# Kernel optimization log

Hardware: AMD Instinct MI355X
Metric: run time of the kernel (lower is better)

Reference implementation:

```python
import jax, jax.numpy as jnp
import numpy as np

B, T, D = 2, 4096, 512
H, W = 8, 32
HD = D // H            # 64
HIDDEN = 3 * D         # SwiGLU expansion = 3
SCALE = float(np.sqrt(HD))
EPS = 1e-5


def setup_inputs() -> dict:
    key = jax.random.key(0)
    ks = jax.random.split(key, 8)
    s = 0.02  # small init for weight matrices
    return {
        "x": jax.random.normal(ks[0], (B, T, D), dtype=jnp.float32),
        "pre_g": jnp.ones((D,), jnp.float32), "pre_b": jnp.zeros((D,), jnp.float32),
        "wq": jax.random.normal(ks[1], (D, D), jnp.float32) * s,
        "wkv": jax.random.normal(ks[2], (D, 2 * D), jnp.float32) * s,
        "wo": jax.random.normal(ks[3], (D, D), jnp.float32) * s,
        "attn_g": jnp.ones((D,), jnp.float32), "attn_b": jnp.zeros((D,), jnp.float32),
        "freqs": jax.random.normal(ks[4], (D,), jnp.float32) * 0.02,
        "phases": jnp.zeros((D,), jnp.float32),
        "amp": jnp.full((1,), 0.1, jnp.float32),
        "w_gate": jax.random.normal(ks[5], (D, HIDDEN), jnp.float32) * s,
        "w_val": jax.random.normal(ks[6], (D, HIDDEN), jnp.float32) * s,
        "w_proj": jax.random.normal(ks[7], (HIDDEN, D), jnp.float32) * s,
        "ffn_g": jnp.ones((D,), jnp.float32), "ffn_b": jnp.zeros((D,), jnp.float32),
    }


def _ln(x, g, b):
    mu = jnp.mean(x, axis=-1, keepdims=True)
    var = jnp.mean(jnp.square(x - mu), axis=-1, keepdims=True)
    return (x - mu) * jax.lax.rsqrt(var + EPS) * g + b


def _gather_window(z):
    # z: (B, T, H, C) -> nb: (B, T, W, H, C) with nb[:, t, w] = z[:, t-1-w] (zeros if t-1-w < 0)
    zp = jnp.pad(z, ((0, 0), (W, 0), (0, 0), (0, 0)))
    idx = jnp.arange(T)[:, None] + (W - 1) - jnp.arange(W)[None, :]  # (T, W), values in [0, T+W-1)
    return zp[:, idx]  # (B, T, W, H, C)


def reference(x, pre_g, pre_b, wq, wkv, wo, attn_g, attn_b,
              freqs, phases, amp, w_gate, w_val, w_proj, ffn_g, ffn_b):
    h = _ln(x, pre_g, pre_b)

    # ---- multi-head causal tension (sigmoid local attention) ----
    q = (h @ wq).reshape(B, T, H, HD)
    kv = (h @ wkv).reshape(B, T, H, 2 * HD)
    nb_kv = _gather_window(kv)                     # (B, T, W, H, 2*HD)
    nb_k, nb_v = nb_kv[..., :HD], nb_kv[..., HD:]
    tau = jax.nn.sigmoid(jnp.einsum('bthd,btwhd->bthw', q, nb_k) / SCALE)
    msg = jnp.einsum('bthw,btwhd->bthd', tau, nb_v).reshape(B, T, D)
    h = _ln(h + msg @ wo, attn_g, attn_b)

    # ---- oscillatory modulation ----
    pos = jnp.arange(T, dtype=jnp.float32)[:, None]  # (T, 1)
    mod = jnp.sin(pos * freqs + phases)              # (T, D)
    y = h * (1.0 + amp * mod)[None]

    # ---- SwiGLU FFN ----
    z = (jax.nn.silu(y @ w_gate) * (y @ w_val)) @ w_proj
    return _ln(y + z, ffn_g, ffn_b)
```

## Files before the change

kernel.cpp:

```cpp
#include <hip/hip_runtime.h>
#include <hip/hip_bf16.h>
#include <math.h>

#define T_LEN   4096
#define D_DIM   512
#define H_NUM   8
#define HD_DIM  64
#define W_WIN   32
#define HID_DIM 1536
#define M_ROWS  8192
#define QKV_LD  1536
#define BK 64

typedef __hip_bfloat16 bf16;
typedef __bf16  bf16x8 __attribute__((ext_vector_type(8)));
typedef float   f32x4  __attribute__((ext_vector_type(4)));

__device__ __forceinline__ float b2f(bf16 x) { return __bfloat162float(x); }
__device__ __forceinline__ bf16  f2b(float x){ return __float2bfloat16(x); }

__device__ __forceinline__ float rdP(const void* p, int i, bool f32) {
  return f32 ? ((const float*)p)[i] : b2f(((const bf16*)p)[i]);
}

__device__ __forceinline__ float wave_reduce_sum(float v) {
  #pragma unroll
  for (int off = 32; off; off >>= 1) v += __shfl_xor(v, off, 64);
  return v;
}

__device__ __forceinline__ bool detect_f32(const unsigned* __restrict__ x) {
  int lane = threadIdx.x & 63;
  int votes = 0;
  #pragma unroll
  for (int i = 0; i < 4; ++i) {
    unsigned e = (x[lane * 4 + i] >> 7) & 0xffu;
    votes += (e >= 90u && e <= 140u) ? 1 : 0;
  }
  float v = wave_reduce_sum((float)votes);
  return v < 200.f;
}

__device__ __forceinline__ void swizzle_xy(int gx, int& bx, int& by) {
  int lid = blockIdx.x;
  int sub = lid & 7;
  int grp = lid >> 3;
  bx = grp % gx;
  by = (grp / gx) * 8 + sub;
}

__global__ __launch_bounds__(256) void ln_kernel(
    const void* __restrict__ in, const void* __restrict__ g, const void* __restrict__ bb,
    void* __restrict__ out, int mode,
    const void* __restrict__ freqs, const void* __restrict__ phases,
    const void* __restrict__ amp,
    const unsigned* __restrict__ xdet, int in_follows, int out_follows)
{
  bool f32  = detect_f32(xdet);
  bool inF  = f32 && (in_follows != 0);
  bool outF = f32 && (out_follows != 0);

  int wave = threadIdx.x >> 6;
  int lane = threadIdx.x & 63;
  int row  = blockIdx.x * 4 + wave;

  float x[8];
  if (inF) {
    const float* rp = (const float*)in + (size_t)row * D_DIM + lane * 8;
    float4 v0 = *reinterpret_cast<const float4*>(rp);
    float4 v1 = *reinterpret_cast<const float4*>(rp + 4);
    x[0]=v0.x; x[1]=v0.y; x[2]=v0.z; x[3]=v0.w;
    x[4]=v1.x; x[5]=v1.y; x[6]=v1.z; x[7]=v1.w;
  } else {
    bf16x8 v = *reinterpret_cast<const bf16x8*>(
        (const bf16*)in + (size_t)row * D_DIM + lane * 8);
    #pragma unroll
    for (int i = 0; i < 8; ++i) x[i] = (float)v[i];
  }

  float s = 0.f, s2 = 0.f;
  #pragma unroll
  for (int i = 0; i < 8; ++i) { s += x[i]; s2 += x[i]*x[i]; }
  s  = wave_reduce_sum(s);
  s2 = wave_reduce_sum(s2);
  float mu   = s * (1.f / D_DIM);
  float var  = s2 * (1.f / D_DIM) - mu * mu;
  float rstd = rsqrtf(var + 1e-5f);

  int t = row & (T_LEN - 1);
  float ampf = (mode == 1) ? rdP(amp, 0, f32) : 0.f;

  float o[8];
  #pragma unroll
  for (int i = 0; i < 8; ++i) {
    int d = lane * 8 + i;
    float val = (x[i] - mu) * rstd * rdP(g, d, f32) + rdP(bb, d, f32);
    if (mode == 1) {
      float m = sinf(fmaf((float)t, rdP(freqs, d, f32), rdP(phases, d, f32)));
      val *= (1.f + ampf * m);
    }
    o[i] = val;
  }

  if (outF) {
    float* op = (float*)out + (size_t)row * D_DIM + lane * 8;
    *reinterpret_cast<float4*>(op)     = make_float4(o[0], o[1], o[2], o[3]);
    *reinterpret_cast<float4*>(op + 4) = make_float4(o[4], o[5], o[6], o[7]);
  } else {
    bf16x8 ov;
    #pragma unroll
    for (int i = 0; i < 8; ++i) ov[i] = (__bf16)o[i];
    *reinterpret_cast<bf16x8*>((bf16*)out + (size_t)row * D_DIM + lane * 8) = ov;
  }
}

__global__ __launch_bounds__(256) void transpose_all_kernel(
    const void* s0, const void* s1, const void* s2, const void* s3,
    const void* s4, const void* s5,
    bf16* d0, bf16* d1, bf16* d2, bf16* d3, bf16* d4, bf16* d5,
    const unsigned* __restrict__ xdet)
{
  bool f32 = detect_f32(xdet);
  int bid = blockIdx.x;
  const void* src; bf16* dst; int R, C, lid, tiles_x;
  if      (bid < 256)  { src=s0; dst=d0; R=512;  C=512;  lid=bid;      tiles_x=16; }
  else if (bid < 768)  { src=s1; dst=d1; R=512;  C=1024; lid=bid-256;  tiles_x=32; }
  else if (bid < 1024) { src=s2; dst=d2; R=512;  C=512;  lid=bid-768;  tiles_x=16; }
  else if (bid < 1792) { src=s3; dst=d3; R=512;  C=1536; lid=bid-1024; tiles_x=48; }
  else if (bid < 2560) { src=s4; dst=d4; R=512;  C=1536; lid=bid-1792; tiles_x=48; }
  else                 { src=s5; dst=d5; R=1536; C=512;  lid=bid-2560; tiles_x=16; }

  __shared__ bf16 tile[32][33];
  int tx = threadIdx.x & 31;
  int ty = threadIdx.x >> 5;
  int c0 = (lid % tiles_x) * 32;
  int r0 = (lid / tiles_x) * 32;
  #pragma unroll
  for (int j = 0; j < 32; j += 8)
    tile[ty + j][tx] = f2b(rdP(src, (size_t)(r0 + ty + j) * C + c0 + tx, f32));
  __syncthreads();
  #pragma unroll
  for (int j = 0; j < 32; j += 8)
    dst[(size_t)(c0 + ty + j) * R + r0 + tx] = tile[tx][ty + j];
}

__global__ __launch_bounds__(256) void gemm64_kernel(
    const bf16* __restrict__ A, const bf16* __restrict__ Bt,
    bf16* Cout, const bf16* extra, int N, int K, int lda, int mode, int gx)
{
  __shared__ alignas(16) bf16 As[64 * BK];
  __shared__ alignas(16) bf16 Bs[64 * BK];

  int bx, by; swizzle_xy(gx, bx, by);
  int mbase = by * 64, nbase = bx * 64;
  int lane = threadIdx.x & 63;
  int wid  = threadIdx.x >> 6;
  int quad = lane >> 4, l16 = lane & 15;
  int wm = (wid >> 1) * 32, wn = (wid & 1) * 32;

  int r0 = wid * 16 + (lane >> 3);
  int cl = lane & 7;
  int cg = cl ^ (lane >> 3);
  const bf16* Ag0 = A  + (size_t)(mbase + r0) * lda + cg * 8;
  const bf16* Ag1 = Ag0 + (size_t)8 * lda;
  const bf16* Bg0 = Bt + (size_t)(nbase + r0) * K + cg * 8;
  const bf16* Bg1 = Bg0 + (size_t)8 * K;

  bf16x8 rA0 = *reinterpret_cast<const bf16x8*>(Ag0);
  bf16x8 rA1 = *reinterpret_cast<const bf16x8*>(Ag1);
  bf16x8 rB0 = *reinterpret_cast<const bf16x8*>(Bg0);
  bf16x8 rB1 = *reinterpret_cast<const bf16x8*>(Bg1);

  f32x4 acc[2][2] = {};

  for (int kleft = K / BK; kleft > 0; --kleft) {
    __syncthreads();
    *reinterpret_cast<bf16x8*>(&As[r0 * BK + cl * 8])       = rA0;
    *reinterpret_cast<bf16x8*>(&As[(r0 + 8) * BK + cl * 8]) = rA1;
    *reinterpret_cast<bf16x8*>(&Bs[r0 * BK + cl * 8])       = rB0;
    *reinterpret_cast<bf16x8*>(&Bs[(r0 + 8) * BK + cl * 8]) = rB1;
    __syncthreads();

    if (kleft > 1) {
      Ag0 += BK; Ag1 += BK; Bg0 += BK; Bg1 += BK;
      rA0 = *reinterpret_cast<const bf16x8*>(Ag0);
      rA1 = *reinterpret_cast<const bf16x8*>(Ag1);
      rB0 = *reinterpret_cast<const bf16x8*>(Bg0);
      rB1 = *reinterpret_cast<const bf16x8*>(Bg1);
    }

    #pragma unroll
    for (int ko = 0; ko < 2; ++ko) {
      bf16x8 a[2], b[2];
      #pragma unroll
      for (int i = 0; i < 2; ++i) {
        int c = (ko * 4 + quad) ^ (l16 & 7);
        a[i] = *reinterpret_cast<const bf16x8*>(&As[(wm + i * 16 + l16) * BK + c * 8]);
        b[i] = *reinterpret_cast<const bf16x8*>(&Bs[(wn + i * 16 + l16) * BK + c * 8]);
      }
      #pragma unroll
      for (int i = 0; i < 2; ++i)
        #pragma unroll
        for (int j = 0; j < 2; ++j)
          acc[i][j] = __builtin_amdgcn_mfma_f32_16x16x32_bf16(a[i], b[j], acc[i][j], 0, 0, 0);
    }
  }

  #pragma unroll
  for (int i = 0; i < 2; ++i)
    #pragma unroll
    for (int j = 0; j < 2; ++j)
      #pragma unroll
      for (int r = 0; r < 4; ++r) {
        int row = mbase + wm + i * 16 + quad * 4 + r;
        int col = nbase + wn + j * 16 + l16;
        size_t idx = (size_t)row * N + col;
        float c = acc[i][j][r];
        if (mode == 1) c += b2f(extra[idx]);
        Cout[idx] = f2b(c);
      }
}

__global__ __launch_bounds__(256) void gateval_kernel(
    const bf16* __restrict__ A, const bf16* __restrict__ Btg,
    const bf16* __restrict__ Btv, bf16* __restrict__ Cout,
    int N, int K, int lda, int gx)
{
  __shared__ alignas(16) bf16 As [64 * BK];
  __shared__ alignas(16) bf16 Bgs[64 * BK];
  __shared__ alignas(16) bf16 Bvs[64 * BK];

  int bx, by; swizzle_xy(gx, bx, by);
  int mbase = by * 64, nbase = bx * 64;
  int lane = threadIdx.x & 63;
  int wid  = threadIdx.x >> 6;
  int quad = lane >> 4, l16 = lane & 15;
  int wm = (wid >> 1) * 32, wn = (wid & 1) * 32;

  int r0 = wid * 16 + (lane >> 3);
  int cl = lane & 7;
  int cg = cl ^ (lane >> 3);
  const bf16* Ag0 = A   + (size_t)(mbase + r0) * lda + cg * 8;
  const bf16* Ag1 = Ag0 + (size_t)8 * lda;
  const bf16* Gg0 = Btg + (size_t)(nbase + r0) * K + cg * 8;
  const bf16* Gg1 = Gg0 + (size_t)8 * K;
  const bf16* Vg0 = Btv + (size_t)(nbase + r0) * K + cg * 8;
  const bf16* Vg1 = Vg0 + (size_t)8 * K;

  bf16x8 rA0 = *reinterpret_cast<const bf16x8*>(Ag0);
  bf16x8 rA1 = *reinterpret_cast<const bf16x8*>(Ag1);
  bf16x8 rG0 = *reinterpret_cast<const bf16x8*>(Gg0);
  bf16x8 rG1 = *reinterpret_cast<const bf16x8*>(Gg1);
  bf16x8 rV0 = *reinterpret_cast<const bf16x8*>(Vg0);
  bf16x8 rV1 = *reinterpret_cast<const bf16x8*>(Vg1);

  f32x4 accg[2][2] = {};
  f32x4 accv[2][2] = {};

  for (int kleft = K / BK; kleft > 0; --kleft) {
    __syncthreads();
    *reinterpret_cast<bf16x8*>(&As [r0 * BK + cl * 8])       = rA0;
    *reinterpret_cast<bf16x8*>(&As [(r0 + 8) * BK + cl * 8]) = rA1;
    *reinterpret_cast<bf16x8*>(&Bgs[r0 * BK + cl * 8])       = rG0;
    *reinterpret_cast<bf16x8*>(&Bgs[(r0 + 8) * BK + cl * 8]) = rG1;
    *reinterpret_cast<bf16x8*>(&Bvs[r0 * BK + cl * 8])       = rV0;
    *reinterpret_cast<bf16x8*>(&Bvs[(r0 + 8) * BK + cl * 8]) = rV1;
    __syncthreads();

    if (kleft > 1) {
      Ag0 += BK; Ag1 += BK; Gg0 += BK; Gg1 += BK; Vg0 += BK; Vg1 += BK;
      rA0 = *reinterpret_cast<const bf16x8*>(Ag0);
      rA1 = *reinterpret_cast<const bf16x8*>(Ag1);
      rG0 = *reinterpret_cast<const bf16x8*>(Gg0);
      rG1 = *reinterpret_cast<const bf16x8*>(Gg1);
      rV0 = *reinterpret_cast<const bf16x8*>(Vg0);
      rV1 = *reinterpret_cast<const bf16x8*>(Vg1);
    }

    #pragma unroll
    for (int ko = 0; ko < 2; ++ko) {
      bf16x8 a[2], bg[2], bv[2];
      #pragma unroll
      for (int i = 0; i < 2; ++i) {
        int c = (ko * 4 + quad) ^ (l16 & 7);
        a[i]  = *reinterpret_cast<const bf16x8*>(&As [(wm + i * 16 + l16) * BK + c * 8]);
        bg[i] = *reinterpret_cast<const bf16x8*>(&Bgs[(wn + i * 16 + l16) * BK + c * 8]);
        bv[i] = *reinterpret_cast<const bf16x8*>(&Bvs[(wn + i * 16 + l16) * BK + c * 8]);
      }
      #pragma unroll
      for (int i = 0; i < 2; ++i)
        #pragma unroll
        for (int j = 0; j < 2; ++j) {
          accg[i][j] = __builtin_amdgcn_mfma_f32_16x16x32_bf16(a[i], bg[j], accg[i][j], 0, 0, 0);
          accv[i][j] = __builtin_amdgcn_mfma_f32_16x16x32_bf16(a[i], bv[j], accv[i][j], 0, 0, 0);
        }
    }
  }

  #pragma unroll
  for (int i = 0; i < 2; ++i)
    #pragma unroll
    for (int j = 0; j < 2; ++j)
      #pragma unroll
      for (int r = 0; r < 4; ++r) {
        int row = mbase + wm + i * 16 + quad * 4 + r;
        int col = nbase + wn + j * 16 + l16;
        float g = accg[i][j][r];
        float v = accv[i][j][r];
        Cout[(size_t)row * N + col] = f2b(g / (1.f + expf(-g)) * v);
      }
}

#define VT_BYTES 9216
#define PL_BYTES 2304
#define ATTN_SET (VT_BYTES + PL_BYTES)
__device__ __forceinline__ int vt_addr(int d, int t) { return d * 144 + t * 2; }

__global__ __launch_bounds__(256) void attn_mfma_kernel(bf16* qkv)
{
  __shared__ alignas(16) char lds_raw[4 * ATTN_SET];
  int lane = threadIdx.x & 63;
  int widx = threadIdx.x >> 6;
  int u    = blockIdx.x * 4 + widx;
  int tile = u >> 3, head = u & 7;
  int rowbase = tile * 16;
  int t0   = rowbase & (T_LEN - 1);
  int l16  = lane & 15, quad = lane >> 4;

  char* wbase = lds_raw + widx * ATTN_SET;
  char* Vl = wbase;
  bf16* Pl = (bf16*)(wbase + VT_BYTES);

  #pragma unroll
  for (int it = 0; it < 6; ++it) {
    int chunk = it * 64 + lane;
    int t  = chunk >> 3;
    int dc = chunk & 7;
    int row = rowbase - 32 + t;
    if (row < 0) row = 0;
    bf16x8 v = *reinterpret_cast<const bf16x8*>(
        qkv + (size_t)row * QKV_LD + 512 + head * 128 + 64 + dc * 8);
    #pragma unroll
    for (int jj = 0; jj < 8; ++jj)
      *(bf16*)(Vl + vt_addr(dc * 8 + jj, t)) = (bf16)(__bf16)v[jj];
  }
  bf16x8 z = {};
  *reinterpret_cast<bf16x8*>(Vl + vt_addr(lane, 48)) = z;
  *reinterpret_cast<bf16x8*>(Vl + vt_addr(lane, 56)) = z;

  bf16x8 aq0, aq1;
  {
    const bf16* qrow = qkv + (size_t)(rowbase + l16) * QKV_LD + head * HD_DIM + quad * 8;
    aq0 = *reinterpret_cast<const bf16x8*>(qrow);
    aq1 = *reinterpret_cast<const bf16x8*>(qrow + 32);
  }

  f32x4 sacc[3] = {};
  #pragma unroll
  for (int jt = 0; jt < 3; ++jt) {
    int tok = rowbase - 32 + jt * 16 + l16;
    if (tok < 0) tok = 0;
    const bf16* krow = qkv + (size_t)tok * QKV_LD + 512 + head * 128 + quad * 8;
    bf16x8 b0 = *reinterpret_cast<const bf16x8*>(krow);
    bf16x8 b1 = *reinterpret_cast<const bf16x8*>(krow + 32);
    sacc[jt] = __builtin_amdgcn_mfma_f32_16x16x32_bf16(aq0, b0, sacc[jt], 0, 0, 0);
    sacc[jt] = __builtin_amdgcn_mfma_f32_16x16x32_bf16(aq1, b1, sacc[jt], 0, 0, 0);
  }

  #pragma unroll
  for (int jt = 0; jt < 3; ++jt) {
    int j = jt * 16 + l16;
    #pragma unroll
    for (int r = 0; r < 4; ++r) {
      int i = quad * 4 + r;
      bool valid = (j >= i) && (j <= i + 31) && (t0 - 32 + j >= 0);
      float tau = valid ? 1.f / (1.f + expf(-sacc[jt][r] * 0.125f)) : 0.f;
      Pl[i * 72 + j] = f2b(tau);
    }
  }
  #pragma unroll
  for (int r = 0; r < 4; ++r) Pl[(quad * 4 + r) * 72 + 48 + l16] = f2b(0.f);

  __syncthreads();

  bf16x8 ap0 = *reinterpret_cast<const bf16x8*>((char*)Pl + l16 * 144 + quad * 16);
  bf16x8 ap1 = *reinterpret_cast<const bf16x8*>((char*)Pl + l16 * 144 + 64 + quad * 16);

  f32x4 macc[4] = {};
  #pragma unroll
  for (int nt = 0; nt < 4; ++nt) {
    int d = nt * 16 + l16;
    bf16x8 bv0 = *reinterpret_cast<const bf16x8*>(Vl + vt_addr(d, quad * 8));
    bf16x8 bv1 = *reinterpret_cast<const bf16x8*>(Vl + vt_addr(d, 32 + quad * 8));
    macc[nt] = __builtin_amdgcn_mfma_f32_16x16x32_bf16(ap0, bv0, macc[nt], 0, 0, 0);
    macc[nt] = __builtin_amdgcn_mfma_f32_16x16x32_bf16(ap1, bv1, macc[nt], 0, 0, 0);
  }

  #pragma unroll
  for (int nt = 0; nt < 4; ++nt)
    #pragma unroll
    for (int r = 0; r < 4; ++r)
      qkv[(size_t)(rowbase + quad * 4 + r) * QKV_LD + head * HD_DIM + nt * 16 + l16] =
          f2b(macc[nt][r]);
}

extern "C" void kernel_launch(void* const* d_in, const int* in_sizes, int n_in,
                              void* d_out, int out_size, void* d_ws, size_t ws_size,
                              hipStream_t stream)
{
  const void* x      = d_in[0];
  const void* pre_g  = d_in[1];
  const void* pre_b  = d_in[2];
  const void* wq     = d_in[3];
  const void* wkv    = d_in[4];
  const void* wo     = d_in[5];
  const void* attn_g = d_in[6];
  const void* attn_b = d_in[7];
  const void* freqs  = d_in[8];
  const void* phases = d_in[9];
  const void* amp    = d_in[10];
  const void* w_gate = d_in[11];
  const void* w_val  = d_in[12];
  const void* w_proj = d_in[13];
  const void* ffn_g  = d_in[14];
  const void* ffn_b  = d_in[15];
  const unsigned* xdet = (const unsigned*)x;

  char* ws = (char*)d_ws;
  bf16* Btqkv = (bf16*)(ws + 512);
  bf16* Bto   = (bf16*)(ws + 1573376);
  bf16* Btg   = (bf16*)(ws + 2097664);
  bf16* Btv   = (bf16*)(ws + 3670528);
  bf16* Btp   = (bf16*)(ws + 5243392);
  bf16* h     = (bf16*)(ws + 6816256);
  bf16* qkvb  = (bf16*)(ws + 15204864);
  bf16* gb    = qkvb;

  transpose_all_kernel<<<3328, 256, 0, stream>>>(
      wq, wkv, wo, w_gate, w_val, w_proj,
      Btqkv, Btqkv + 512 * 512, Bto, Btg, Btv, Btp, xdet);

  ln_kernel<<<2048, 256, 0, stream>>>(x, pre_g, pre_b, h, 0,
                                      nullptr, nullptr, nullptr, xdet, 1, 0);

  gemm64_kernel<<<3072, 256, 0, stream>>>(h, Btqkv, qkvb, nullptr,
                                          1536, 512, 512, 0, 24);

  attn_mfma_kernel<<<1024, 256, 0, stream>>>(qkvb);

  gemm64_kernel<<<1024, 256, 0, stream>>>(qkvb, Bto, h, h,
                                          512, 512, QKV_LD, 1, 8);

  ln_kernel<<<2048, 256, 0, stream>>>(h, attn_g, attn_b, h, 1,
                                      freqs, phases, amp, xdet, 0, 0);

  gateval_kernel<<<3072, 256, 0, stream>>>(h, Btg, Btv, gb,
                                           1536, 512, 512, 24);

  gemm64_kernel<<<1024, 256, 0, stream>>>(gb, Btp, h, h,
                                          512, 1536, QKV_LD, 1, 8);

  ln_kernel<<<2048, 256, 0, stream>>>(h, ffn_g, ffn_b, d_out, 0,
                                      nullptr, nullptr, nullptr, xdet, 0, 1);
}
```

Baseline: 292.6 us.

## Enlarge GEMM tiles to 128-row blocks and load via direct global-to-LDS

The GEMM and gate/value kernels now use 128-row M tiles, and 128-wide N tiles for the QKV projection, so each wave computes a larger accumulator block. This gives more MFMA reuse per shared-memory load and launches fewer blocks. Tiles are staged with global_load_lds (buffer-to-LDS direct loads) instead of register prefetch followed by LDS stores. The register-level prefetch overlap is dropped, so global loads are no longer hidden behind the previous tile's MFMAs. Larger accumulators and LDS use may also lower occupancy.

```diff
diff --git a/kernel.cpp b/kernel.cpp
--- a/kernel.cpp
+++ b/kernel.cpp
@@ -16,8 +16,16 @@
 typedef __bf16  bf16x8 __attribute__((ext_vector_type(8)));
 typedef float   f32x4  __attribute__((ext_vector_type(4)));
 
+#define G_AS __attribute__((address_space(1)))
+#define L_AS __attribute__((address_space(3)))
+
 __device__ __forceinline__ float b2f(bf16 x) { return __bfloat162float(x); }
 __device__ __forceinline__ bf16  f2b(float x){ return __float2bfloat16(x); }
+
+__device__ __forceinline__ void gload_lds16(const bf16* g, bf16* l) {
+  __builtin_amdgcn_global_load_lds((const G_AS unsigned int*)g,
+                                   (L_AS unsigned int*)l, 16, 0, 0);
+}
 
 __device__ __forceinline__ float rdP(const void* p, int i, bool f32) {
   return f32 ? ((const float*)p)[i] : b2f(((const bf16*)p)[i]);
@@ -144,80 +152,71 @@
     dst[(size_t)(c0 + ty + j) * R + r0 + tx] = tile[tx][ty + j];
 }
 
-__global__ __launch_bounds__(256) void gemm64_kernel(
+template<int BNT>
+__global__ __launch_bounds__(256) void gemm_tile_kernel(
     const bf16* __restrict__ A, const bf16* __restrict__ Bt,
     bf16* Cout, const bf16* extra, int N, int K, int lda, int mode, int gx)
 {
-  __shared__ alignas(16) bf16 As[64 * BK];
-  __shared__ alignas(16) bf16 Bs[64 * BK];
+  constexpr int BJ = BNT / 32;
+  __shared__ alignas(16) bf16 As[128 * BK];
+  __shared__ alignas(16) bf16 Bs[BNT * BK];
 
   int bx, by; swizzle_xy(gx, bx, by);
-  int mbase = by * 64, nbase = bx * 64;
-  int lane = threadIdx.x & 63;
-  int wid  = threadIdx.x >> 6;
+  int mbase = by * 128, nbase = bx * BNT;
+  int tid  = threadIdx.x;
+  int lane = tid & 63;
+  int wid  = tid >> 6;
   int quad = lane >> 4, l16 = lane & 15;
-  int wm = (wid >> 1) * 32, wn = (wid & 1) * 32;
-
-  int r0 = wid * 16 + (lane >> 3);
-  int cl = lane & 7;
-  int cg = cl ^ (lane >> 3);
-  const bf16* Ag0 = A  + (size_t)(mbase + r0) * lda + cg * 8;
-  const bf16* Ag1 = Ag0 + (size_t)8 * lda;
-  const bf16* Bg0 = Bt + (size_t)(nbase + r0) * K + cg * 8;
-  const bf16* Bg1 = Bg0 + (size_t)8 * K;
-
-  bf16x8 rA0 = *reinterpret_cast<const bf16x8*>(Ag0);
-  bf16x8 rA1 = *reinterpret_cast<const bf16x8*>(Ag1);
-  bf16x8 rB0 = *reinterpret_cast<const bf16x8*>(Bg0);
-  bf16x8 rB1 = *reinterpret_cast<const bf16x8*>(Bg1);
-
-  f32x4 acc[2][2] = {};
+  int wm = (wid >> 1) * 64, wn = (wid & 1) * (BNT / 2);
+
+  int srow = tid >> 3;
+  int scol = (tid & 7) ^ (srow & 7);
+  const bf16* Ag = A  + (size_t)(mbase + srow) * lda + scol * 8;
+  const bf16* Bg = Bt + (size_t)(nbase + srow) * K   + scol * 8;
+
+  f32x4 acc[4][BJ] = {};
 
   for (int kleft = K / BK; kleft > 0; --kleft) {
     __syncthreads();
-    *reinterpret_cast<bf16x8*>(&As[r0 * BK + cl * 8])       = rA0;
-    *reinterpret_cast<bf16x8*>(&As[(r0 + 8) * BK + cl * 8]) = rA1;
-    *reinterpret_cast<bf16x8*>(&Bs[r0 * BK + cl * 8])       = rB0;
-    *reinterpret_cast<bf16x8*>(&Bs[(r0 + 8) * BK + cl * 8]) = rB1;
+    #pragma unroll
+    for (int j = 0; j < 4; ++j)
+      gload_lds16(Ag + (size_t)(j * 32) * lda, &As[j * 2048 + tid * 8]);
+    #pragma unroll
+    for (int j = 0; j < BJ; ++j)
+      gload_lds16(Bg + (size_t)(j * 32) * K,   &Bs[j * 2048 + tid * 8]);
+    Ag += BK; Bg += BK;
     __syncthreads();
 
-    if (kleft > 1) {
-      Ag0 += BK; Ag1 += BK; Bg0 += BK; Bg1 += BK;
-      rA0 = *reinterpret_cast<const bf16x8*>(Ag0);
-      rA1 = *reinterpret_cast<const bf16x8*>(Ag1);
-      rB0 = *reinterpret_cast<const bf16x8*>(Bg0);
-      rB1 = *reinterpret_cast<const bf16x8*>(Bg1);
-    }
-
     #pragma unroll
     for (int ko = 0; ko < 2; ++ko) {
-      bf16x8 a[2], b[2];
-      #pragma unroll
-      for (int i = 0; i < 2; ++i) {
-        int c = (ko * 4 + quad) ^ (l16 & 7);
-        a[i] = *reinterpret_cast<const bf16x8*>(&As[(wm + i * 16 + l16) * BK + c * 8]);
-        b[i] = *reinterpret_cast<const bf16x8*>(&Bs[(wn + i * 16 + l16) * BK + c * 8]);
-      }
-      #pragma unroll
-      for (int i = 0; i < 2; ++i)
+      bf16x8 a[4], b[BJ];
+      int c = ((ko * 4 + quad) ^ (l16 & 7)) * 8;
+      #pragma unroll
+      for (int i = 0; i < 4; ++i)
+        a[i] = *reinterpret_cast<const bf16x8*>(&As[(wm + i * 16 + l16) * BK + c]);
+      #pragma unroll
+      for (int j = 0; j < BJ; ++j)
+        b[j] = *reinterpret_cast<const bf16x8*>(&Bs[(wn + j * 16 + l16) * BK + c]);
+      #pragma unroll
+      for (int i = 0; i < 4; ++i)
         #pragma unroll
-        for (int j = 0; j < 2; ++j)
+        for (int j = 0; j < BJ; ++j)
           acc[i][j] = __builtin_amdgcn_mfma_f32_16x16x32_bf16(a[i], b[j], acc[i][j], 0, 0, 0);
     }
   }
 
   #pragma unroll
-  for (int i = 0; i < 2; ++i)
-    #pragma unroll
-    for (int j = 0; j < 2; ++j)
+  for (int i = 0; i < 4; ++i)
+    #pragma unroll
+    for (int j = 0; j < BJ; ++j)
       #pragma unroll
       for (int r = 0; r < 4; ++r) {
         int row = mbase + wm + i * 16 + quad * 4 + r;
         int col = nbase + wn + j * 16 + l16;
         size_t idx = (size_t)row * N + col;
-        float c = acc[i][j][r];
-        if (mode == 1) c += b2f(extra[idx]);
-        Cout[idx] = f2b(c);
+        float cv = acc[i][j][r];
+        if (mode == 1) cv += b2f(extra[idx]);
+        Cout[idx] = f2b(cv);
       }
 }
 
@@ -226,69 +225,54 @@
     const bf16* __restrict__ Btv, bf16* __restrict__ Cout,
     int N, int K, int lda, int gx)
 {
-  __shared__ alignas(16) bf16 As [64 * BK];
-  __shared__ alignas(16) bf16 Bgs[64 * BK];
-  __shared__ alignas(16) bf16 Bvs[64 * BK];
+  __shared__ alignas(16) bf16 As [128 * BK];
+  __shared__ alignas(16) bf16 Bgs[ 64 * BK];
+  __shared__ alignas(16) bf16 Bvs[ 64 * BK];
 
   int bx, by; swizzle_xy(gx, bx, by);
-  int mbase = by * 64, nbase = bx * 64;
-  int lane = threadIdx.x & 63;
-  int wid  = threadIdx.x >> 6;
+  int mbase = by * 128, nbase = bx * 64;
+  int tid  = threadIdx.x;
+  int lane = tid & 63;
+  int wid  = tid >> 6;
   int quad = lane >> 4, l16 = lane & 15;
-  int wm = (wid >> 1) * 32, wn = (wid & 1) * 32;
-
-  int r0 = wid * 16 + (lane >> 3);
-  int cl = lane & 7;
-  int cg = cl ^ (lane >> 3);
-  const bf16* Ag0 = A   + (size_t)(mbase + r0) * lda + cg * 8;
-  const bf16* Ag1 = Ag0 + (size_t)8 * lda;
-  const bf16* Gg0 = Btg + (size_t)(nbase + r0) * K + cg * 8;
-  const bf16* Gg1 = Gg0 + (size_t)8 * K;
-  const bf16* Vg0 = Btv + (size_t)(nbase + r0) * K + cg * 8;
-  const bf16* Vg1 = Vg0 + (size_t)8 * K;
-
-  bf16x8 rA0 = *reinterpret_cast<const bf16x8*>(Ag0);
-  bf16x8 rA1 = *reinterpret_cast<const bf16x8*>(Ag1);
-  bf16x8 rG0 = *reinterpret_cast<const bf16x8*>(Gg0);
-  bf16x8 rG1 = *reinterpret_cast<const bf16x8*>(Gg1);
-  bf16x8 rV0 = *reinterpret_cast<const bf16x8*>(Vg0);
-  bf16x8 rV1 = *reinterpret_cast<const bf16x8*>(Vg1);
-
-  f32x4 accg[2][2] = {};
-  f32x4 accv[2][2] = {};
+  int wm = (wid >> 1) * 64, wn = (wid & 1) * 32;
+
+  int srow = tid >> 3;
+  int scol = (tid & 7) ^ (srow & 7);
+  const bf16* Ag = A   + (size_t)(mbase + srow) * lda + scol * 8;
+  const bf16* Gg = Btg + (size_t)(nbase + srow) * K   + scol * 8;
+  const bf16* Vg = Btv + (size_t)(nbase + srow) * K   + scol * 8;
+
+  f32x4 accg[4][2] = {};
+  f32x4 accv[4][2] = {};
 
   for (int kleft = K / BK; kleft > 0; --kleft) {
     __syncthreads();
-    *reinterpret_cast<bf16x8*>(&As [r0 * BK + cl * 8])       = rA0;
-    *reinterpret_cast<bf16x8*>(&As [(r0 + 8) * BK + cl * 8]) = rA1;
-    *reinterpret_cast<bf16x8*>(&Bgs[r0 * BK + cl * 8])       = rG0;
-    *reinterpret_cast<bf16x8*>(&Bgs[(r0 + 8) * BK + cl * 8]) = rG1;
-    *reinterpret_cast<bf16x8*>(&Bvs[r0 * BK + cl * 8])       = rV0;
-    *reinterpret_cast<bf16x8*>(&Bvs[(r0 + 8) * BK + cl * 8]) = rV1;
+    #pragma unroll
+    for (int j = 0; j < 4; ++j)
+      gload_lds16(Ag + (size_t)(j * 32) * lda, &As[j * 2048 + tid * 8]);
+    #pragma unroll
+    for (int j = 0; j < 2; ++j) {
+      gload_lds16(Gg + (size_t)(j * 32) * K, &Bgs[j * 2048 + tid * 8]);
+      gload_lds16(Vg + (size_t)(j * 32) * K, &Bvs[j * 2048 + tid * 8]);
+    }
+    Ag += BK; Gg += BK; Vg += BK;
     __syncthreads();
 
-    if (kleft > 1) {
-      Ag0 += BK; Ag1 += BK; Gg0 += BK; Gg1 += BK; Vg0 += BK; Vg1 += BK;
-      rA0 = *reinterpret_cast<const bf16x8*>(Ag0);
-      rA1 = *reinterpret_cast<const bf16x8*>(Ag1);
-      rG0 = *reinterpret_cast<const bf16x8*>(Gg0);
-      rG1 = *reinterpret_cast<const bf16x8*>(Gg1);
-      rV0 = *reinterpret_cast<const bf16x8*>(Vg0);
-      rV1 = *reinterpret_cast<const bf16x8*>(Vg1);
-    }
-
     #pragma unroll
     for (int ko = 0; ko < 2; ++ko) {
-      bf16x8 a[2], bg[2], bv[2];
-      #pragma unroll
-      for (int i = 0; i < 2; ++i) {
-        int c = (ko * 4 + quad) ^ (l16 & 7);
-        a[i]  = *reinterpret_cast<const bf16x8*>(&As [(wm + i * 16 + l16) * BK + c * 8]);
-        bg[i] = *reinterpret_cast<const bf16x8*>(&Bgs[(wn + i * 16 + l16) * BK + c * 8]);
-        bv[i] = *reinterpret_cast<const bf16x8*>(&Bvs[(wn + i * 16 + l16) * BK + c * 8]);
+      bf16x8 a[4], bg[2], bv[2];
+      int c = ((ko * 4 + quad) ^ (l16 & 7)) * 8;
+      #pragma unroll
+      for (int i = 0; i < 4; ++i)
+        a[i]  = *reinterpret_cast<const bf16x8*>(&As [(wm + i * 16 + l16) * BK + c]);
+      #pragma unroll
+      for (int j = 0; j < 2; ++j) {
+        bg[j] = *reinterpret_cast<const bf16x8*>(&Bgs[(wn + j * 16 + l16) * BK + c]);
+        bv[j] = *reinterpret_cast<const bf16x8*>(&Bvs[(wn + j * 16 + l16) * BK + c]);
       }
       #pragma unroll
-      for (int i = 0; i < 2; ++i)
+      for (int i = 0; i < 4; ++i)
         #pragma unroll
         for (int j = 0; j < 2; ++j) {
           accg[i][j] = __builtin_amdgcn_mfma_f32_16x16x32_bf16(a[i], bg[j], accg[i][j], 0, 0, 0);
@@ -298,7 +282,7 @@
   }
 
   #pragma unroll
-  for (int i = 0; i < 2; ++i)
+  for (int i = 0; i < 4; ++i)
     #pragma unroll
     for (int j = 0; j < 2; ++j)
       #pragma unroll
@@ -443,22 +427,22 @@
   ln_kernel<<<2048, 256, 0, stream>>>(x, pre_g, pre_b, h, 0,
                                       nullptr, nullptr, nullptr, xdet, 1, 0);
 
-  gemm64_kernel<<<3072, 256, 0, stream>>>(h, Btqkv, qkvb, nullptr,
-                                          1536, 512, 512, 0, 24);
+  gemm_tile_kernel<128><<<768, 256, 0, stream>>>(h, Btqkv, qkvb, nullptr,
+                                                 1536, 512, 512, 0, 12);
 
   attn_mfma_kernel<<<1024, 256, 0, stream>>>(qkvb);
 
-  gemm64_kernel<<<1024, 256, 0, stream>>>(qkvb, Bto, h, h,
-                                          512, 512, QKV_LD, 1, 8);
+  gemm_tile_kernel<64><<<512, 256, 0, stream>>>(qkvb, Bto, h, h,
+                                                512, 512, QKV_LD, 1, 8);
 
   ln_kernel<<<2048, 256, 0, stream>>>(h, attn_g, attn_b, h, 1,
                                       freqs, phases, amp, xdet, 0, 0);
 
-  gateval_kernel<<<3072, 256, 0, stream>>>(h, Btg, Btv, gb,
+  gateval_kernel<<<1536, 256, 0, stream>>>(h, Btg, Btv, gb,
                                            1536, 512, 512, 24);
 
-  gemm64_kernel<<<1024, 256, 0, stream>>>(gb, Btp, h, h,
-                                          512, 1536, QKV_LD, 1, 8);
+  gemm_tile_kernel<64><<<512, 256, 0, stream>>>(gb, Btp, h, h,
+                                                512, 1536, QKV_LD, 1, 8);
 
   ln_kernel<<<2048, 256, 0, stream>>>(h, ffn_g, ffn_b, d_out, 0,
                                       nullptr, nullptr, nullptr, xdet, 0, 1);
```

New measurement: 298.9 us. 2.2% more time.
